# Optimization experiments

Measured on AMD Instinct MI355X. Metric: run time of the kernel, lower is better.

Reference implementation:

```python
import jax, jax.numpy as jnp
import numpy as np

B_, S_, D_, N_, R_ = 2, 2048, 1024, 16, 64  # batch, seq, d_model, d_state, dt_rank


def setup_inputs() -> dict:
    key = jax.random.key(0)
    ks = jax.random.split(key, 12)
    x = jax.random.normal(ks[0], (B_, S_, D_), dtype=jnp.float32)
    # params (xavier-ish scale)
    W_dtw = jax.random.normal(ks[1], (R_, D_), dtype=jnp.float32) * (1.0 / np.sqrt(D_))
    W_dt = jax.random.normal(ks[2], (D_, R_), dtype=jnp.float32) * (1.0 / np.sqrt(R_))
    b_dt = jnp.zeros((D_,), dtype=jnp.float32)
    A_log = jnp.log(jax.random.uniform(ks[3], (D_, N_), minval=0.5, maxval=1.5, dtype=jnp.float32))
    W_B = jax.random.normal(ks[4], (N_, D_), dtype=jnp.float32) * (1.0 / np.sqrt(D_))
    W_C = jax.random.normal(ks[5], (N_, D_), dtype=jnp.float32) * (1.0 / np.sqrt(D_))
    Dp = jnp.ones((D_,), dtype=jnp.float32)
    ln_g = jnp.ones((D_,), dtype=jnp.float32)
    ln_b = jnp.zeros((D_,), dtype=jnp.float32)
    W_out = jax.random.normal(ks[6], (D_, D_), dtype=jnp.float32) * (1.0 / np.sqrt(D_))
    return {"x": x, "W_dtw": W_dtw, "W_dt": W_dt, "b_dt": b_dt, "A_log": A_log,
            "W_B": W_B, "W_C": W_C, "Dp": Dp, "ln_g": ln_g, "ln_b": ln_b, "W_out": W_out}


def _layernorm(y, g, b, eps=1e-5):
    mu = jnp.mean(y, axis=-1, keepdims=True)
    var = jnp.mean(jnp.square(y - mu), axis=-1, keepdims=True)
    return (y - mu) * jax.lax.rsqrt(var + eps) * g + b


def reference(x, W_dtw, W_dt, b_dt, A_log, W_B, W_C, Dp, ln_g, ln_b, W_out):
    # projections
    dt = jnp.einsum('bsd,rd->bsr', x, W_dtw)                 # [B,S,R]
    delta = jax.nn.softplus(jnp.einsum('bsr,dr->bsd', dt, W_dt) + b_dt)  # [B,S,D]
    Bm = jnp.einsum('bsd,nd->bsn', x, W_B)                   # [B,S,N]
    Cm = jnp.einsum('bsd,nd->bsn', x, W_C)                   # [B,S,N]
    A = -jnp.exp(A_log)                                      # [D,N]

    def step(h, inp):
        d_t, b_t, c_t, x_t = inp                             # [B,D],[B,N],[B,N],[B,D]
        dA = jnp.exp(d_t[..., None] * A)                     # [B,D,N]
        h = dA * h + (d_t[..., None] * b_t[:, None, :]) * x_t[..., None]
        y_t = jnp.sum(h * c_t[:, None, :], axis=-1)          # [B,D]
        return h, y_t

    h0 = jnp.zeros((x.shape[0], x.shape[2], A.shape[1]), dtype=x.dtype)
    xs = (jnp.swapaxes(delta, 0, 1), jnp.swapaxes(Bm, 0, 1),
          jnp.swapaxes(Cm, 0, 1), jnp.swapaxes(x, 0, 1))
    _, ys = jax.lax.scan(step, h0, xs)                       # ys: [S,B,D]
    y = jnp.swapaxes(ys, 0, 1) + Dp * x                      # [B,S,D]
    y = _layernorm(y, ln_g, ln_b)
    return jnp.einsum('bsd,ed->bse', y, W_out)
```

## Files before the change

### kernel.cpp

```cpp
#include <hip/hip_runtime.h>
#include <hip/hip_bf16.h>

#define B_ 2
#define S_ 2048
#define D_ 1024
#define N_ 16
#define R_ 64
#define NC 64
#define CL 32
#define BS_ (B_*S_)

typedef __attribute__((ext_vector_type(4))) float f32x4;
typedef __attribute__((ext_vector_type(8))) short bf16x8;
typedef __attribute__((ext_vector_type(8))) unsigned short u16x8;

__device__ __forceinline__ unsigned short f2b(float v) {
  unsigned u = __builtin_bit_cast(unsigned, v);
  unsigned r = ((u >> 16) & 1u) + 0x7FFFu;
  return (unsigned short)((u + r) >> 16);
}

__device__ __forceinline__ void gload_lds16(const void* g, void* l) {
  __builtin_amdgcn_global_load_lds(
      (const __attribute__((address_space(1))) unsigned int*)g,
      (__attribute__((address_space(3))) unsigned int*)l, 16, 0, 0);
}

__global__ __launch_bounds__(256) void k_castall(
    const float* __restrict__ x, const float* __restrict__ W_B,
    const float* __restrict__ W_C, const float* __restrict__ W_dt,
    const float* __restrict__ W_out, const float* __restrict__ W_dtw,
    unsigned short* __restrict__ xb, unsigned short* __restrict__ WBC,
    unsigned short* __restrict__ wdtb, unsigned short* __restrict__ wob,
    unsigned short* __restrict__ wdtwT) {
  int i = (blockIdx.x * 256 + threadIdx.x) * 4;
  if (i < 5341184) {
    const float* s; unsigned short* d; int off;
    if (i < 4194304)      { s = x;     d = xb;          off = 0; }
    else if (i < 4210688) { s = W_B;   d = WBC;         off = 4194304; }
    else if (i < 4227072) { s = W_C;   d = WBC + 16384; off = 4210688; }
    else if (i < 4292608) { s = W_dt;  d = wdtb;        off = 4227072; }
    else                  { s = W_out; d = wob;         off = 4292608; }
    int j = i - off;
    float4 v = *(const float4*)&s[j];
    ushort4 o;
    o.x = f2b(v.x); o.y = f2b(v.y); o.z = f2b(v.z); o.w = f2b(v.w);
    *(ushort4*)&d[j] = o;
  } else {
    int j = i - 5341184;
    int r = j >> 10, e = j & 1023;
    float4 v = *(const float4*)&W_dtw[j];
    wdtwT[(size_t)(e + 0) * 64 + r] = f2b(v.x);
    wdtwT[(size_t)(e + 1) * 64 + r] = f2b(v.y);
    wdtwT[(size_t)(e + 2) * 64 + r] = f2b(v.z);
    wdtwT[(size_t)(e + 3) * 64 + r] = f2b(v.w);
  }
}

__global__ __launch_bounds__(256) void k_weff(
    const unsigned short* __restrict__ wdtb, const unsigned short* __restrict__ wdtwT,
    unsigned short* __restrict__ weff) {
  __shared__ __align__(16) unsigned short As[128 * 64];
  __shared__ __align__(16) unsigned short Bs[128 * 64];
  const int tid = threadIdx.x;
  const int lane = tid & 63, wid = tid >> 6;
  const int wr = wid >> 1, wc = wid & 1;
  const size_t row0 = (size_t)blockIdx.x * 128;
  const size_t col0 = (size_t)blockIdx.y * 128;
  f32x4 acc[4][4] = {};
  {
    const int r = tid >> 3, s = tid & 7;
    #pragma unroll
    for (int i = 0; i < 4; ++i) {
      const int row = i * 32 + r;
      const int gs = s ^ (row & 7);
      gload_lds16(wdtb + (row0 + row) * R_ + gs * 8, As + row * 64 + s * 8);
      gload_lds16(wdtwT + (col0 + row) * R_ + gs * 8, Bs + row * 64 + s * 8);
    }
  }
  __syncthreads();
  const int r = lane & 15, kg = lane >> 4;
  #pragma unroll
  for (int ks = 0; ks < 2; ++ks) {
    bf16x8 a[4], b[4];
    #pragma unroll
    for (int m = 0; m < 4; ++m) {
      const int arow = wr * 64 + m * 16 + r;
      a[m] = *(const bf16x8*)&As[arow * 64 + (((ks << 2) | kg) ^ (arow & 7)) * 8];
    }
    #pragma unroll
    for (int n = 0; n < 4; ++n) {
      const int brow = wc * 64 + n * 16 + r;
      b[n] = *(const bf16x8*)&Bs[brow * 64 + (((ks << 2) | kg) ^ (brow & 7)) * 8];
    }
    #pragma unroll
    for (int m = 0; m < 4; ++m)
      #pragma unroll
      for (int n = 0; n < 4; ++n)
        acc[m][n] = __builtin_amdgcn_mfma_f32_16x16x32_bf16(a[m], b[n], acc[m][n], 0, 0, 0);
  }
  const int cr = lane >> 4, cc = lane & 15;
  #pragma unroll
  for (int m = 0; m < 4; ++m)
    #pragma unroll
    for (int n = 0; n < 4; ++n)
      #pragma unroll
      for (int j = 0; j < 4; ++j)
        weff[(row0 + wr * 64 + m * 16 + cr * 4 + j) * D_ + col0 + wc * 64 + n * 16 + cc]
            = f2b(acc[m][n][j]);
}

__device__ __forceinline__ void stage128x64(const unsigned short* __restrict__ g,
                                            size_t row0, int k0,
                                            unsigned short* lds, int tid) {
  const int r = tid >> 3, s = tid & 7;
  #pragma unroll
  for (int i = 0; i < 4; ++i) {
    const int row = i * 32 + r;
    const int gs = s ^ (row & 7);
    gload_lds16(g + ((row0 + row) << 10) + k0 + (gs << 3), lds + row * 64 + s * 8);
  }
}

__device__ __forceinline__ void stage64x64(const unsigned short* __restrict__ g,
                                           size_t row0, int k0,
                                           unsigned short* lds, int tid) {
  const int r = tid >> 3, s = tid & 7;
  #pragma unroll
  for (int i = 0; i < 2; ++i) {
    const int row = i * 32 + r;
    const int gs = s ^ (row & 7);
    gload_lds16(g + ((row0 + row) << 10) + k0 + (gs << 3), lds + row * 64 + s * 8);
  }
}

__global__ __launch_bounds__(256, 2) void k_deltaBC(
    const unsigned short* __restrict__ xb, const unsigned short* __restrict__ weff,
    const unsigned short* __restrict__ WBC, const float* __restrict__ b_dt,
    float* __restrict__ delta, float* __restrict__ Bm, float* __restrict__ Cm) {
  __shared__ __align__(16) unsigned short As[2][128 * 64];
  __shared__ __align__(16) unsigned short Bs[2][64 * 64];
  const int tid = threadIdx.x;
  const int lane = tid & 63, wid = tid >> 6;
  const size_t row0 = (size_t)blockIdx.x * 128;
  const int by = blockIdx.y;
  const bool bc = (by == 16);
  f32x4 acc[2][4] = {};

  auto stageB = [&](int buf, int k0) {
    if (!bc) {
      stage64x64(weff, (size_t)by * 64, k0, Bs[buf], tid);
    } else {
      const int row = tid >> 3, s = tid & 7;
      const int gs = s ^ (row & 7);
      gload_lds16(WBC + (size_t)row * D_ + k0 + (gs << 3), Bs[buf] + row * 64 + s * 8);
    }
  };

  stage128x64(xb, row0, 0, As[0], tid);
  stageB(0, 0);
  __syncthreads();

  int cur = 0;
  const int r = lane & 15, kg = lane >> 4;
  for (int t = 0; t < 16; ++t) {
    if (t + 1 < 16) {
      stage128x64(xb, row0, (t + 1) * 64, As[cur ^ 1], tid);
      stageB(cur ^ 1, (t + 1) * 64);
    }
    if (!bc) {
      #pragma unroll
      for (int ks = 0; ks < 2; ++ks) {
        bf16x8 a[2], b[4];
        #pragma unroll
        for (int m = 0; m < 2; ++m) {
          const int arow = wid * 32 + m * 16 + r;
          a[m] = *(const bf16x8*)&As[cur][arow * 64 + (((ks << 2) | kg) ^ (arow & 7)) * 8];
        }
        #pragma unroll
        for (int n = 0; n < 4; ++n) {
          const int brow = n * 16 + r;
          b[n] = *(const bf16x8*)&Bs[cur][brow * 64 + (((ks << 2) | kg) ^ (brow & 7)) * 8];
        }
        #pragma unroll
        for (int m = 0; m < 2; ++m)
          #pragma unroll
          for (int n = 0; n < 4; ++n)
            acc[m][n] = __builtin_amdgcn_mfma_f32_16x16x32_bf16(a[m], b[n], acc[m][n], 0, 0, 0);
      }
    } else {
      #pragma unroll
      for (int ks = 0; ks < 2; ++ks) {
        bf16x8 a[2], b[2];
        #pragma unroll
        for (int m = 0; m < 2; ++m) {
          const int arow = wid * 32 + m * 16 + r;
          a[m] = *(const bf16x8*)&As[cur][arow * 64 + (((ks << 2) | kg) ^ (arow & 7)) * 8];
        }
        #pragma unroll
        for (int n = 0; n < 2; ++n) {
          const int brow = n * 16 + r;
          b[n] = *(const bf16x8*)&Bs[cur][brow * 64 + (((ks << 2) | kg) ^ (brow & 7)) * 8];
        }
        #pragma unroll
        for (int m = 0; m < 2; ++m)
          #pragma unroll
          for (int n = 0; n < 2; ++n)
            acc[m][n] = __builtin_amdgcn_mfma_f32_16x16x32_bf16(a[m], b[n], acc[m][n], 0, 0, 0);
      }
    }
    __syncthreads();
    cur ^= 1;
  }

  const int cr = lane >> 4, cc = lane & 15;
  if (!bc) {
    #pragma unroll
    for (int m = 0; m < 2; ++m) {
      #pragma unroll
      for (int n = 0; n < 4; ++n) {
        const int d = by * 64 + n * 16 + cc;
        const float bd = b_dt[d];
        #pragma unroll
        for (int j = 0; j < 4; ++j) {
          size_t trow = row0 + wid * 32 + m * 16 + cr * 4 + j;
          float v = acc[m][n][j] + bd;
          float sp = fmaxf(v, 0.f) + log1pf(__expf(-fabsf(v)));
          delta[trow * D_ + d] = sp;
        }
      }
    }
  } else {
    #pragma unroll
    for (int m = 0; m < 2; ++m) {
      #pragma unroll
      for (int n = 0; n < 2; ++n) {
        const int col = n * 16 + cc;
        #pragma unroll
        for (int j = 0; j < 4; ++j) {
          size_t trow = row0 + wid * 32 + m * 16 + cr * 4 + j;
          float v = acc[m][n][j];
          if (col < 16) Bm[trow * N_ + col] = v;
          else          Cm[trow * N_ + col - 16] = v;
        }
      }
    }
  }
}

__global__ __launch_bounds__(256) void k_scan1(
    const float* __restrict__ x, const float* __restrict__ delta,
    const float* __restrict__ Bm, const float* __restrict__ A_log,
    float* __restrict__ sdsum, float* __restrict__ hend) {
  __shared__ __align__(16) float sd[CL][64];
  __shared__ __align__(16) float sx[CL][64];
  __shared__ __align__(16) float sB[CL][N_];
  const int tid = threadIdx.x;
  const int db = blockIdx.x & 15;
  const int c  = (blockIdx.x >> 4) & (NC - 1);
  const int b  = blockIdx.x >> 10;
  const int d0 = db * 64;
  const size_t tokbase = (size_t)(b * S_ + c * CL);

  {
    int s = tid >> 4, jf = (tid & 15) * 4;
    size_t g = (tokbase + s) * D_ + d0 + jf;
    gload_lds16(&delta[g], &sd[s][jf]);
    gload_lds16(&x[g],     &sx[s][jf]);
    gload_lds16(&delta[g + (size_t)16 * D_], &sd[s + 16][jf]);
    gload_lds16(&x[g + (size_t)16 * D_],     &sx[s + 16][jf]);
    if (tid < 128) {
      int s2 = tid >> 2, nf = (tid & 3) * 4;
      gload_lds16(&Bm[(tokbase + s2) * N_ + nf], &sB[s2][nf]);
    }
  }
  const int nq = tid & 3, dl = tid >> 2;
  const int d = d0 + dl;
  float4 av = *(const float4*)&A_log[(size_t)d * N_ + nq * 4];
  float Ad0 = -__expf(av.x), Ad1 = -__expf(av.y);
  float Ad2 = -__expf(av.z), Ad3 = -__expf(av.w);
  __syncthreads();

  float sds = 0.f;
  float h0 = 0.f, h1 = 0.f, h2 = 0.f, h3 = 0.f;
  #pragma unroll 8
  for (int s = 0; s < CL; ++s) {
    float dlt = sd[s][dl];
    float dbx = dlt * sx[s][dl];
    sds += dlt;
    float4 Bv = *(const float4*)&sB[s][nq * 4];
    float da0 = __expf(dlt * Ad0), da1 = __expf(dlt * Ad1);
    float da2 = __expf(dlt * Ad2), da3 = __expf(dlt * Ad3);
    h0 = da0 * h0 + dbx * Bv.x;
    h1 = da1 * h1 + dbx * Bv.y;
    h2 = da2 * h2 + dbx * Bv.z;
    h3 = da3 * h3 + dbx * Bv.w;
  }
  size_t o = (((size_t)(b * NC + c)) * D_ + d) * N_ + nq * 4;
  *(float4*)&hend[o] = make_float4(h0, h1, h2, h3);
  if (nq == 0) sdsum[(size_t)(b * NC + c) * D_ + d] = sds;
}

__global__ __launch_bounds__(256) void k_scan2(
    const float* __restrict__ sdsum, const float* __restrict__ hend,
    const float* __restrict__ A_log, float* __restrict__ hstart) {
  int g = blockIdx.x * 256 + threadIdx.x;
  int n = g & (N_ - 1);
  int d = (g >> 4) & (D_ - 1);
  int b = g >> 14;
  float Ad = -__expf(A_log[(size_t)d * N_ + n]);
  float h = 0.f;
  for (int c = 0; c < NC; ++c) {
    size_t idx = (((size_t)b * NC + c) * D_ + d) * N_ + n;
    float ap = __expf(Ad * sdsum[(size_t)(b * NC + c) * D_ + d]);
    hstart[idx] = h;
    h = ap * h + hend[idx];
  }
}

__global__ __launch_bounds__(256) void k_scan3(
    const float* __restrict__ x, const float* __restrict__ delta,
    const float* __restrict__ Bm, const float* __restrict__ Cm,
    const float* __restrict__ A_log, const float* __restrict__ hstart,
    const float* __restrict__ Dp, float* __restrict__ ypre) {
  __shared__ __align__(16) float sd[CL][64];
  __shared__ __align__(16) float sx[CL][64];
  __shared__ __align__(16) float sB[CL][N_];
  __shared__ __align__(16) float sC[CL][N_];
  __shared__ __align__(16) float sy[CL][64];
  const int tid = threadIdx.x;
  const int db = blockIdx.x & 15;
  const int c  = (blockIdx.x >> 4) & (NC - 1);
  const int b  = blockIdx.x >> 10;
  const int d0 = db * 64;
  const size_t tokbase = (size_t)(b * S_ + c * CL);

  {
    int s = tid >> 4, jf = (tid & 15) * 4;
    size_t g = (tokbase + s) * D_ + d0 + jf;
    gload_lds16(&delta[g], &sd[s][jf]);
    gload_lds16(&x[g],     &sx[s][jf]);
    gload_lds16(&delta[g + (size_t)16 * D_], &sd[s + 16][jf]);
    gload_lds16(&x[g + (size_t)16 * D_],     &sx[s + 16][jf]);
    if (tid < 128) {
      int s2 = tid >> 2, nf = (tid & 3) * 4;
      gload_lds16(&Bm[(tokbase + s2) * N_ + nf], &sB[s2][nf]);
      gload_lds16(&Cm[(tokbase + s2) * N_ + nf], &sC[s2][nf]);
    }
  }
  const int nq = tid & 3, dl = tid >> 2;
  const int d = d0 + dl;
  float4 av = *(const float4*)&A_log[(size_t)d * N_ + nq * 4];
  float Ad0 = -__expf(av.x), Ad1 = -__expf(av.y);
  float Ad2 = -__expf(av.z), Ad3 = -__expf(av.w);
  float h0, h1, h2, h3;
  {
    size_t o = (((size_t)(b * NC + c)) * D_ + d) * N_ + nq * 4;
    float4 v = *(const float4*)&hstart[o];
    h0 = v.x; h1 = v.y; h2 = v.z; h3 = v.w;
  }
  const float Dpd = Dp[d];
  __syncthreads();

  #pragma unroll 8
  for (int s = 0; s < CL; ++s) {
    float dlt = sd[s][dl];
    float xv  = sx[s][dl];
    float dbx = dlt * xv;
    float4 Bv = *(const float4*)&sB[s][nq * 4];
    float4 Cv = *(const float4*)&sC[s][nq * 4];
    float da0 = __expf(dlt * Ad0), da1 = __expf(dlt * Ad1);
    float da2 = __expf(dlt * Ad2), da3 = __expf(dlt * Ad3);
    h0 = da0 * h0 + dbx * Bv.x;
    h1 = da1 * h1 + dbx * Bv.y;
    h2 = da2 * h2 + dbx * Bv.z;
    h3 = da3 * h3 + dbx * Bv.w;
    float y = h0 * Cv.x + h1 * Cv.y + h2 * Cv.z + h3 * Cv.w;
    y += __shfl_xor(y, 1);
    y += __shfl_xor(y, 2);
    if (nq == 0) sy[s][dl] = y + Dpd * xv;
  }
  __syncthreads();
  {
    int s = tid >> 3, j = (tid & 7) * 8;
    size_t g = (tokbase + s) * D_ + d0 + j;
    *(float4*)&ypre[g]     = *(float4*)&sy[s][j];
    *(float4*)&ypre[g + 4] = *(float4*)&sy[s][j + 4];
  }
}

__device__ __forceinline__ float block_sum256(float v, float* sm) {
  #pragma unroll
  for (int o = 32; o > 0; o >>= 1) v += __shfl_down(v, o, 64);
  int w = threadIdx.x >> 6;
  __syncthreads();
  if ((threadIdx.x & 63) == 0) sm[w] = v;
  __syncthreads();
  return (sm[0] + sm[1]) + (sm[2] + sm[3]);
}

__global__ __launch_bounds__(256) void k_ln(
    const float* __restrict__ ypre, const float* __restrict__ g,
    const float* __restrict__ bta, unsigned short* __restrict__ ybf) {
  __shared__ float sm[4];
  const int t = blockIdx.x;
  const int tid = threadIdx.x;
  size_t base = (size_t)t * D_ + tid * 4;
  float4 v = *(const float4*)&ypre[base];
  float s1 = block_sum256(v.x + v.y + v.z + v.w, sm);
  float mu = s1 * (1.f / D_);
  float cx = v.x - mu, cy = v.y - mu, cz = v.z - mu, cw = v.w - mu;
  float s2 = block_sum256(cx*cx + cy*cy + cz*cz + cw*cw, sm);
  float rs = rsqrtf(s2 * (1.f / D_) + 1e-5f);
  float4 gg = *(const float4*)&g[tid * 4];
  float4 bb = *(const float4*)&bta[tid * 4];
  ushort4 o;
  o.x = f2b(cx * rs * gg.x + bb.x);
  o.y = f2b(cy * rs * gg.y + bb.y);
  o.z = f2b(cz * rs * gg.z + bb.z);
  o.w = f2b(cw * rs * gg.w + bb.w);
  *(ushort4*)&ybf[base] = o;
}

__global__ __launch_bounds__(256, 2) void k_out(const unsigned short* __restrict__ Y,
                                                const unsigned short* __restrict__ W,
                                                float* __restrict__ O) {
  __shared__ __align__(16) unsigned short As[2][128 * 64];
  __shared__ __align__(16) unsigned short Bs[2][64 * 64];
  const int tid = threadIdx.x;
  const int lane = tid & 63, wid = tid >> 6;
  const size_t row0 = (size_t)blockIdx.x * 128;
  const size_t col0 = (size_t)blockIdx.y * 64;
  f32x4 acc[2][4] = {};

  stage128x64(Y, row0, 0, As[0], tid);
  stage64x64(W, col0, 0, Bs[0], tid);
  __syncthreads();

  int cur = 0;
  const int r = lane & 15, kg = lane >> 4;
  for (int t = 0; t < 16; ++t) {
    if (t + 1 < 16) {
      stage128x64(Y, row0, (t + 1) * 64, As[cur ^ 1], tid);
      stage64x64(W, col0, (t + 1) * 64, Bs[cur ^ 1], tid);
    }
    #pragma unroll
    for (int ks = 0; ks < 2; ++ks) {
      bf16x8 a[2], b[4];
      #pragma unroll
      for (int m = 0; m < 2; ++m) {
        const int arow = wid * 32 + m * 16 + r;
        a[m] = *(const bf16x8*)&As[cur][arow * 64 + (((ks << 2) | kg) ^ (arow & 7)) * 8];
      }
      #pragma unroll
      for (int n = 0; n < 4; ++n) {
        const int brow = n * 16 + r;
        b[n] = *(const bf16x8*)&Bs[cur][brow * 64 + (((ks << 2) | kg) ^ (brow & 7)) * 8];
      }
      #pragma unroll
      for (int m = 0; m < 2; ++m)
        #pragma unroll
        for (int n = 0; n < 4; ++n)
          acc[m][n] = __builtin_amdgcn_mfma_f32_16x16x32_bf16(a[m], b[n], acc[m][n], 0, 0, 0);
    }
    __syncthreads();
    cur ^= 1;
  }

  const int cr = lane >> 4, cc = lane & 15;
  #pragma unroll
  for (int m = 0; m < 2; ++m) {
    #pragma unroll
    for (int n = 0; n < 4; ++n) {
      size_t orow = row0 + wid * 32 + m * 16 + cr * 4;
      float* op = O + orow * D_ + col0 + n * 16 + cc;
      #pragma unroll
      for (int j = 0; j < 4; ++j) op[(size_t)j * D_] = acc[m][n][j];
    }
  }
}

extern "C" void kernel_launch(void* const* d_in, const int* in_sizes, int n_in,
                              void* d_out, int out_size, void* d_ws, size_t ws_size,
                              hipStream_t stream) {
  const float* x     = (const float*)d_in[0];
  const float* W_dtw = (const float*)d_in[1];
  const float* W_dt  = (const float*)d_in[2];
  const float* b_dt  = (const float*)d_in[3];
  const float* A_log = (const float*)d_in[4];
  const float* W_B   = (const float*)d_in[5];
  const float* W_C   = (const float*)d_in[6];
  const float* Dp    = (const float*)d_in[7];
  const float* ln_g  = (const float*)d_in[8];
  const float* ln_b  = (const float*)d_in[9];
  const float* W_out = (const float*)d_in[10];
  float* out = (float*)d_out;

  float* ws = (float*)d_ws;
  float* delta  = ws;
  float* ypre   = delta  + (size_t)BS_ * D_;
  float* Bm     = ypre   + (size_t)BS_ * D_;
  float* Cm     = Bm     + (size_t)BS_ * N_;
  float* hend   = Cm     + (size_t)BS_ * N_;
  float* hstart = hend   + (size_t)B_ * NC * D_ * N_;
  float* sdsum  = hstart + (size_t)B_ * NC * D_ * N_;
  unsigned short* xb    = (unsigned short*)(sdsum + (size_t)B_ * NC * D_);
  unsigned short* WBC   = xb    + (size_t)BS_ * D_;
  unsigned short* wdtb  = WBC   + (size_t)32 * D_;
  unsigned short* wdtwT = wdtb  + (size_t)D_ * R_;
  unsigned short* weff  = wdtwT + (size_t)D_ * R_;
  unsigned short* wob   = weff  + (size_t)D_ * D_;
  unsigned short* ybf   = wob   + (size_t)D_ * D_;

  k_castall<<<dim3(5280), dim3(256), 0, stream>>>(x, W_B, W_C, W_dt, W_out, W_dtw,
                                                  xb, WBC, wdtb, wob, wdtwT);
  k_weff<<<dim3(8, 8), dim3(256), 0, stream>>>(wdtb, wdtwT, weff);
  k_deltaBC<<<dim3(BS_ / 128, 17), dim3(256), 0, stream>>>(xb, weff, WBC, b_dt,
                                                           delta, Bm, Cm);
  k_scan1<<<dim3(B_ * NC * (D_ / 64)), dim3(256), 0, stream>>>(x, delta, Bm, A_log,
                                                               sdsum, hend);
  k_scan2<<<dim3(B_ * D_ * N_ / 256), dim3(256), 0, stream>>>(sdsum, hend, A_log, hstart);
  k_scan3<<<dim3(B_ * NC * (D_ / 64)), dim3(256), 0, stream>>>(x, delta, Bm, Cm,
                                                               A_log, hstart, Dp, ypre);
  k_ln<<<dim3(BS_), dim3(256), 0, stream>>>(ypre, ln_g, ln_b, ybf);
  k_out<<<dim3(BS_ / 128, D_ / 64), dim3(256), 0, stream>>>(ybf, wob, out);
}
```

Baseline: 113.8 us.

## Widen deltaBC GEMM tile to 128x128 and parallelize chunk scan across lanes

The delta projection GEMM now uses a 128x128 output tile per block with a 2x2 wave layout, halving the grid's y-dimension (9 instead of 17) and raising per-wave MFMA work and operand reuse. The second-stage chunk scan is restructured so 8 lanes split the 64 chunks, each composes a local (A,H) pair, and lanes combine prefixes via shuffles before writing hstart. The scan change turns a 64-step serial loop per thread into 8-step loops plus a short shuffle combine, increasing parallelism at the cost of more threads. The larger GEMM tile uses more LDS and registers per block, which may lower occupancy.

```diff
diff --git a/kernel.cpp b/kernel.cpp
--- a/kernel.cpp
+++ b/kernel.cpp
@@ -139,17 +139,17 @@
     const unsigned short* __restrict__ WBC, const float* __restrict__ b_dt,
     float* __restrict__ delta, float* __restrict__ Bm, float* __restrict__ Cm) {
   __shared__ __align__(16) unsigned short As[2][128 * 64];
-  __shared__ __align__(16) unsigned short Bs[2][64 * 64];
+  __shared__ __align__(16) unsigned short Bs[2][128 * 64];
   const int tid = threadIdx.x;
   const int lane = tid & 63, wid = tid >> 6;
   const size_t row0 = (size_t)blockIdx.x * 128;
   const int by = blockIdx.y;
-  const bool bc = (by == 16);
-  f32x4 acc[2][4] = {};
+  const bool bc = (by == 8);
+  f32x4 acc[4][4] = {};
 
   auto stageB = [&](int buf, int k0) {
     if (!bc) {
-      stage64x64(weff, (size_t)by * 64, k0, Bs[buf], tid);
+      stage128x64(weff, (size_t)by * 128, k0, Bs[buf], tid);
     } else {
       const int row = tid >> 3, s = tid & 7;
       const int gs = s ^ (row & 7);
@@ -169,21 +169,22 @@
       stageB(cur ^ 1, (t + 1) * 64);
     }
     if (!bc) {
+      const int wr = wid >> 1, wc = wid & 1;
       #pragma unroll
       for (int ks = 0; ks < 2; ++ks) {
-        bf16x8 a[2], b[4];
-        #pragma unroll
-        for (int m = 0; m < 2; ++m) {
-          const int arow = wid * 32 + m * 16 + r;
+        bf16x8 a[4], b[4];
+        #pragma unroll
+        for (int m = 0; m < 4; ++m) {
+          const int arow = wr * 64 + m * 16 + r;
           a[m] = *(const bf16x8*)&As[cur][arow * 64 + (((ks << 2) | kg) ^ (arow & 7)) * 8];
         }
         #pragma unroll
         for (int n = 0; n < 4; ++n) {
-          const int brow = n * 16 + r;
+          const int brow = wc * 64 + n * 16 + r;
           b[n] = *(const bf16x8*)&Bs[cur][brow * 64 + (((ks << 2) | kg) ^ (brow & 7)) * 8];
         }
         #pragma unroll
-        for (int m = 0; m < 2; ++m)
+        for (int m = 0; m < 4; ++m)
           #pragma unroll
           for (int n = 0; n < 4; ++n)
             acc[m][n] = __builtin_amdgcn_mfma_f32_16x16x32_bf16(a[m], b[n], acc[m][n], 0, 0, 0);
@@ -215,15 +216,16 @@
 
   const int cr = lane >> 4, cc = lane & 15;
   if (!bc) {
-    #pragma unroll
-    for (int m = 0; m < 2; ++m) {
+    const int wr = wid >> 1, wc = wid & 1;
+    #pragma unroll
+    for (int m = 0; m < 4; ++m) {
       #pragma unroll
       for (int n = 0; n < 4; ++n) {
-        const int d = by * 64 + n * 16 + cc;
+        const int d = by * 128 + wc * 64 + n * 16 + cc;
         const float bd = b_dt[d];
         #pragma unroll
         for (int j = 0; j < 4; ++j) {
-          size_t trow = row0 + wid * 32 + m * 16 + cr * 4 + j;
+          size_t trow = row0 + wr * 64 + m * 16 + cr * 4 + j;
           float v = acc[m][n][j] + bd;
           float sp = fmaxf(v, 0.f) + log1pf(__expf(-fabsf(v)));
           delta[trow * D_ + d] = sp;
@@ -304,17 +306,40 @@
 __global__ __launch_bounds__(256) void k_scan2(
     const float* __restrict__ sdsum, const float* __restrict__ hend,
     const float* __restrict__ A_log, float* __restrict__ hstart) {
-  int g = blockIdx.x * 256 + threadIdx.x;
-  int n = g & (N_ - 1);
-  int d = (g >> 4) & (D_ - 1);
-  int b = g >> 14;
-  float Ad = -__expf(A_log[(size_t)d * N_ + n]);
+  const int tid = threadIdx.x;
+  const int o  = tid & 7;
+  const int n  = (tid >> 3) & 15;
+  const int dl = tid >> 7;
+  const int d2 = blockIdx.x & 511;
+  const int b  = blockIdx.x >> 9;
+  const int d  = d2 * 2 + dl;
+  const float Ad = -__expf(A_log[(size_t)d * N_ + n]);
+
+  float ap8[8], he8[8];
+  float A_loc = 1.f, H_loc = 0.f;
+  #pragma unroll
+  for (int k = 0; k < 8; ++k) {
+    const int c = o * 8 + k;
+    float sds = sdsum[(size_t)(b * NC + c) * D_ + d];
+    float ap = __expf(Ad * sds);
+    float he = hend[((size_t)(b * NC + c) * D_ + d) * N_ + n];
+    ap8[k] = ap; he8[k] = he;
+    A_loc *= ap;
+    H_loc = ap * H_loc + he;
+  }
   float h = 0.f;
-  for (int c = 0; c < NC; ++c) {
-    size_t idx = (((size_t)b * NC + c) * D_ + d) * N_ + n;
-    float ap = __expf(Ad * sdsum[(size_t)(b * NC + c) * D_ + d]);
-    hstart[idx] = h;
-    h = ap * h + hend[idx];
+  const int gb = (tid & 63) & ~7;
+  #pragma unroll
+  for (int j = 0; j < 7; ++j) {
+    float Aj = __shfl(A_loc, gb | j, 64);
+    float Hj = __shfl(H_loc, gb | j, 64);
+    if (o > j) h = Aj * h + Hj;
+  }
+  #pragma unroll
+  for (int k = 0; k < 8; ++k) {
+    const int c = o * 8 + k;
+    hstart[((size_t)(b * NC + c) * D_ + d) * N_ + n] = h;
+    h = ap8[k] * h + he8[k];
   }
 }
 
@@ -515,11 +540,11 @@
   k_castall<<<dim3(5280), dim3(256), 0, stream>>>(x, W_B, W_C, W_dt, W_out, W_dtw,
                                                   xb, WBC, wdtb, wob, wdtwT);
   k_weff<<<dim3(8, 8), dim3(256), 0, stream>>>(wdtb, wdtwT, weff);
-  k_deltaBC<<<dim3(BS_ / 128, 17), dim3(256), 0, stream>>>(xb, weff, WBC, b_dt,
-                                                           delta, Bm, Cm);
+  k_deltaBC<<<dim3(BS_ / 128, 9), dim3(256), 0, stream>>>(xb, weff, WBC, b_dt,
+                                                          delta, Bm, Cm);
   k_scan1<<<dim3(B_ * NC * (D_ / 64)), dim3(256), 0, stream>>>(x, delta, Bm, A_log,
                                                                sdsum, hend);
-  k_scan2<<<dim3(B_ * D_ * N_ / 256), dim3(256), 0, stream>>>(sdsum, hend, A_log, hstart);
+  k_scan2<<<dim3(B_ * (D_ / 2)), dim3(256), 0, stream>>>(sdsum, hend, A_log, hstart);
   k_scan3<<<dim3(B_ * NC * (D_ / 64)), dim3(256), 0, stream>>>(x, delta, Bm, Cm,
                                                                A_log, hstart, Dp, ypre);
   k_ln<<<dim3(BS_), dim3(256), 0, stream>>>(ypre, ln_g, ln_b, ybf);
```

Measured after the change: 119.2 us. +4.8%, slower.
